# Optimization experiments

Hardware: AMD Instinct MI355X
Metric: run time of the kernel (lower is better)

## Reference

```python
import jax, jax.numpy as jnp
import numpy as np

HEADS = 8
DIM_HEAD = 64
INNER = HEADS * DIM_HEAD  # 512
DIM = 256
MSA_H = 128  # number of MSA rows
MSA_W = 256  # sequence length


def setup_inputs() -> dict:
    key = jax.random.key(0)
    ks = jax.random.split(key, 8)
    n = MSA_H * MSA_W
    w_std = 0.02
    return {
        "x": jax.random.normal(ks[0], (1, n, DIM), dtype=jnp.float32),
        "wq_w": jax.random.normal(ks[1], (DIM, INNER), dtype=jnp.float32) * w_std,
        "wkv_w": jax.random.normal(ks[2], (DIM, 2 * INNER), dtype=jnp.float32) * w_std,
        "wout_w": jax.random.normal(ks[3], (INNER, DIM), dtype=jnp.float32) * w_std,
        "wout_b": jnp.zeros((DIM,), dtype=jnp.float32),
        "hq_w": jax.random.normal(ks[4], (DIM, INNER), dtype=jnp.float32) * w_std,
        "hkv_w": jax.random.normal(ks[5], (DIM, 2 * INNER), dtype=jnp.float32) * w_std,
        "hout_w": jax.random.normal(ks[6], (INNER, DIM), dtype=jnp.float32) * w_std,
        "hout_b": jnp.zeros((DIM,), dtype=jnp.float32),
        "msa_h": MSA_H,
        "msa_w": MSA_W,
    }


def reference(x, wq_w, wkv_w, wout_w, wout_b, hq_w, hkv_w, hout_w, hout_b, msa_h, msa_w):
    b, n, d = x.shape
    h, w = msa_h, msa_w
    scale = DIM_HEAD ** -0.5
    x4 = x.reshape(b, h, w, d)  # (b, rows, cols, dim)

    # ---- width attention: attend across MSA rows (h), independent per column (w) ----
    xw = jnp.swapaxes(x4, 1, 2)  # (b, w, h, d)
    q = (xw @ wq_w).reshape(b, w, h, HEADS, DIM_HEAD)
    kv = (xw @ wkv_w).reshape(b, w, h, 2, HEADS, DIM_HEAD)
    k, v = kv[..., 0, :, :], kv[..., 1, :, :]
    dots = jnp.einsum('bwiHd,bwjHd->bwHij', q, k) * scale  # (b, w, H, h, h)
    attn = jax.nn.softmax(dots, axis=-1)
    o = jnp.einsum('bwHij,bwjHd->bwiHd', attn, v).reshape(b, w, h, INNER)
    w_out = o @ wout_w + wout_b  # (b, w, h, d)
    w_out = jnp.swapaxes(w_out, 1, 2)  # (b, h, w, d)

    # ---- height attention: attend across columns (w), rows tied (tie_attn_dim = h) ----
    q = (x4 @ hq_w).reshape(b, h, w, HEADS, DIM_HEAD)
    kv = (x4 @ hkv_w).reshape(b, h, w, 2, HEADS, DIM_HEAD)
    k, v = kv[..., 0, :, :], kv[..., 1, :, :]
    tie_scale = scale * (h ** -0.5)
    # scores summed over tied row dim r: 'b r h i d, b r h j d -> b h i j'
    dots = jnp.einsum('briHd,brjHd->bHij', q, k) * tie_scale  # (b, H, w, w)
    attn = jax.nn.softmax(dots, axis=-1)
    o = jnp.einsum('bHij,brjHd->briHd', attn, v).reshape(b, h, w, INNER)
    h_out = o @ hout_w + hout_b  # (b, h, w, d)

    out = w_out + h_out
    return out.reshape(b, h * w, d)
```

## Files before the change

kernel.cpp:

```cpp
#include <hip/hip_runtime.h>

typedef short s16x8 __attribute__((ext_vector_type(8)));
typedef float f32x4 __attribute__((ext_vector_type(4)));

#define MFMA16(a, b, c) __builtin_amdgcn_mfma_f32_16x16x32_bf16((a), (b), (c), 0, 0, 0)

__device__ __forceinline__ unsigned short f2b(float f) {
  union { float f; unsigned int u; } v; v.f = f;
  unsigned int u = v.u;
  unsigned int r = (u + 0x7fffu + ((u >> 16) & 1u)) >> 16;
  return (unsigned short)r;
}
__device__ __forceinline__ float b2f(unsigned short b) {
  union { unsigned int u; float f; } v; v.u = ((unsigned int)b) << 16;
  return v.f;
}

__device__ __forceinline__ void gld_lds16(const void* g, void* l) {
  __builtin_amdgcn_global_load_lds(
      (const __attribute__((address_space(1))) unsigned int*)g,
      (__attribute__((address_space(3))) unsigned int*)l, 16, 0, 0);
}

__global__ __launch_bounds__(256) void cvt_x(const float* __restrict__ x,
                                             unsigned short* __restrict__ xb) {
  size_t i = ((size_t)blockIdx.x * 256 + threadIdx.x) * 4;
  float4 v = *(const float4*)(x + i);
  ushort4 o;
  o.x = f2b(v.x); o.y = f2b(v.y); o.z = f2b(v.z); o.w = f2b(v.w);
  *(ushort4*)(xb + i) = o;
}

__global__ __launch_bounds__(256) void build_wt(const float* __restrict__ wq,
                                                const float* __restrict__ wkv,
                                                const float* __restrict__ hq,
                                                const float* __restrict__ hkv,
                                                unsigned short* __restrict__ WT) {
  const int n = blockIdx.x, k = threadIdx.x;
  float v;
  if (n < 512)       v = wq [(size_t)k * 512  + n];
  else if (n < 1536) v = wkv[(size_t)k * 1024 + (n - 512)];
  else if (n < 2048) v = hq [(size_t)k * 512  + (n - 1536)];
  else               v = hkv[(size_t)k * 1024 + (n - 2048)];
  WT[(size_t)n * 256 + k] = f2b(v);
}

__global__ __launch_bounds__(256) void build_w2t(const float* __restrict__ wout,
                                                 const float* __restrict__ hout,
                                                 unsigned short* __restrict__ W2T) {
  const int n = blockIdx.x;
  for (int k = threadIdx.x; k < 1024; k += 256) {
    const float v = (k < 512) ? wout[(size_t)k * 256 + n] : hout[(size_t)(k - 512) * 256 + n];
    W2T[(size_t)n * 1024 + k] = f2b(v);
  }
}

__global__ __launch_bounds__(256) void gemm_qkv(const unsigned short* __restrict__ X,
                                                const unsigned short* __restrict__ WT,
                                                unsigned short* __restrict__ C,
                                                int branch) {
  __shared__ unsigned short As[128 * 32];
  __shared__ unsigned short Bs[128 * 32];
  const int tid = threadIdx.x, wave = tid >> 6, lane = tid & 63;
  const int q = lane >> 4, l = lane & 15;
  const int m0 = blockIdx.x * 128;
  const int n0 = blockIdx.y * 128;
  const int mt = (wave >> 1) * 64;
  const int nt = (wave & 1) * 64;
  const char* Xb = (const char*)X;
  const char* Wb = (const char*)WT;
  const int srow = wave * 32 + (lane >> 2);
  const int sboff = (lane & 3) * 16;
  char* AsB = (char*)As;
  char* BsB = (char*)Bs;
  f32x4 acc[4][4] = {};
#pragma unroll
  for (int ks = 0; ks < 8; ++ks) {
    const int kb = ks * 64;
    gld_lds16(Xb + (size_t)(m0 + srow) * 512 + kb + sboff, AsB + wave * 2048);
    gld_lds16(Xb + (size_t)(m0 + srow + 16) * 512 + kb + sboff, AsB + wave * 2048 + 1024);
    gld_lds16(Wb + (size_t)(n0 + srow) * 512 + kb + sboff, BsB + wave * 2048);
    gld_lds16(Wb + (size_t)(n0 + srow + 16) * 512 + kb + sboff, BsB + wave * 2048 + 1024);
    __syncthreads();
    s16x8 a[4], b[4];
#pragma unroll
    for (int i = 0; i < 4; ++i) a[i] = *(const s16x8*)(&As[(mt + i * 16 + l) * 32 + q * 8]);
#pragma unroll
    for (int j = 0; j < 4; ++j) b[j] = *(const s16x8*)(&Bs[(nt + j * 16 + l) * 32 + q * 8]);
#pragma unroll
    for (int i = 0; i < 4; ++i)
#pragma unroll
      for (int j = 0; j < 4; ++j) acc[i][j] = MFMA16(a[i], b[j], acc[i][j]);
    __syncthreads();
  }
#pragma unroll
  for (int i = 0; i < 4; ++i)
#pragma unroll
    for (int j = 0; j < 4; ++j) {
      const int col = n0 + nt + j * 16 + l;
      const int part = col >> 9, H = (col & 511) >> 6, d = col & 63;
      unsigned short* base = C + (size_t)part * 16777216;
#pragma unroll
      for (int r = 0; r < 4; ++r) {
        const int m = m0 + mt + i * 16 + q * 4 + r;
        size_t idx;
        if (branch == 0) idx = ((size_t)((m & 255) * 8 + H) * 128 + (m >> 8)) * 64 + d;
        else             idx = ((size_t)((m >> 8) * 8 + H) * 256 + (m & 255)) * 64 + d;
        base[idx] = f2b(acc[i][j][r]);
      }
    }
}

__global__ __launch_bounds__(256) void col_attn(const unsigned short* __restrict__ C,
                                                unsigned short* __restrict__ O) {
  __shared__ unsigned short Sp[128 * 136];
  __shared__ unsigned short Vt[64 * 136];
  __shared__ float rowinv[128];
  const int w = blockIdx.x, H = blockIdx.y;
  const int tid = threadIdx.x, wave = tid >> 6, lane = tid & 63;
  const int q = lane >> 4, l = lane & 15;
  const size_t slab = (size_t)(w * 8 + H) * 8192;
  const unsigned short* Qs = C + slab;
  const unsigned short* Ks = C + 16777216 + slab;
  const unsigned short* Vs = C + 33554432 + slab;
  for (int u = tid; u < 1024; u += 256) {
    const int j = u >> 3, db = u & 7;
    s16x8 v = *(const s16x8*)(Vs + j * 64 + db * 8);
#pragma unroll
    for (int t = 0; t < 8; ++t) Vt[(db * 8 + t) * 136 + j] = v[t];
  }
  {
    const int m0 = wave * 32;
    f32x4 acc[2][8] = {};
#pragma unroll
    for (int ks = 0; ks < 2; ++ks) {
      const int kk = ks * 32 + q * 8;
      s16x8 a[2], b[8];
#pragma unroll
      for (int i = 0; i < 2; ++i) a[i] = *(const s16x8*)(Qs + (m0 + i * 16 + l) * 64 + kk);
#pragma unroll
      for (int j = 0; j < 8; ++j) b[j] = *(const s16x8*)(Ks + (j * 16 + l) * 64 + kk);
#pragma unroll
      for (int i = 0; i < 2; ++i)
#pragma unroll
        for (int j = 0; j < 8; ++j) acc[i][j] = MFMA16(a[i], b[j], acc[i][j]);
    }
#pragma unroll
    for (int i = 0; i < 2; ++i)
#pragma unroll
      for (int j = 0; j < 8; ++j)
#pragma unroll
        for (int r = 0; r < 4; ++r)
          Sp[(m0 + i * 16 + q * 4 + r) * 136 + j * 16 + l] = f2b(acc[i][j][r] * 0.125f);
  }
  __syncthreads();
  if (tid < 128) {
    float mx = -1e30f;
    for (int j = 0; j < 128; ++j) mx = fmaxf(mx, b2f(Sp[tid * 136 + j]));
    float s = 0.f;
    for (int j = 0; j < 128; ++j) {
      float e = __expf(b2f(Sp[tid * 136 + j]) - mx);
      s += e;
      Sp[tid * 136 + j] = f2b(e);
    }
    rowinv[tid] = 1.0f / s;
  }
  __syncthreads();
  {
    const int m0 = wave * 32;
    f32x4 acc[2][4] = {};
#pragma unroll
    for (int ks = 0; ks < 4; ++ks) {
      const int kk = ks * 32 + q * 8;
      s16x8 a[2], b[4];
#pragma unroll
      for (int i = 0; i < 2; ++i) a[i] = *(const s16x8*)(&Sp[(m0 + i * 16 + l) * 136 + kk]);
#pragma unroll
      for (int j = 0; j < 4; ++j) b[j] = *(const s16x8*)(&Vt[(j * 16 + l) * 136 + kk]);
#pragma unroll
      for (int i = 0; i < 2; ++i)
#pragma unroll
        for (int j = 0; j < 4; ++j) acc[i][j] = MFMA16(a[i], b[j], acc[i][j]);
    }
#pragma unroll
    for (int i = 0; i < 2; ++i)
#pragma unroll
      for (int j = 0; j < 4; ++j)
#pragma unroll
        for (int r = 0; r < 4; ++r) {
          const int row = m0 + i * 16 + q * 4 + r;
          const int d = j * 16 + l;
          O[(size_t)(row * 256 + w) * 1024 + H * 64 + d] = f2b(acc[i][j][r] * rowinv[row]);
        }
  }
}

__global__ __launch_bounds__(256) void row_dots(const unsigned short* __restrict__ C,
                                                float* __restrict__ dp) {
  const int H = blockIdx.z;
  const int r0 = blockIdx.y * 16;
  const int ti = blockIdx.x & 1, tj = blockIdx.x >> 1;
  const int tid = threadIdx.x, wave = tid >> 6, lane = tid & 63;
  const int q = lane >> 4, l = lane & 15;
  const int m0 = ti * 128 + (wave >> 1) * 64;
  const int n0 = tj * 128 + (wave & 1) * 64;
  const unsigned short* Qh = C;
  const unsigned short* Kh = C + 16777216;
  f32x4 acc[4][4] = {};
  for (int ks = 0; ks < 32; ++ks) {
    const int k = ks * 32 + q * 8;
    const int rr = r0 + (k >> 6), d = k & 63;
    const size_t slab = (size_t)(rr * 8 + H) * 16384;
    s16x8 a[4], b[4];
#pragma unroll
    for (int i = 0; i < 4; ++i) a[i] = *(const s16x8*)(Qh + slab + (m0 + i * 16 + l) * 64 + d);
#pragma unroll
    for (int j = 0; j < 4; ++j) b[j] = *(const s16x8*)(Kh + slab + (n0 + j * 16 + l) * 64 + d);
#pragma unroll
    for (int i = 0; i < 4; ++i)
#pragma unroll
      for (int j = 0; j < 4; ++j) acc[i][j] = MFMA16(a[i], b[j], acc[i][j]);
  }
  float* outp = dp + ((size_t)blockIdx.y * 8 + H) * 65536;
#pragma unroll
  for (int i = 0; i < 4; ++i)
#pragma unroll
    for (int j = 0; j < 4; ++j)
#pragma unroll
      for (int r = 0; r < 4; ++r)
        outp[(size_t)(m0 + i * 16 + q * 4 + r) * 256 + n0 + j * 16 + l] = acc[i][j][r];
}

__global__ __launch_bounds__(256) void row_softmax(const float* __restrict__ dp,
                                                   unsigned short* __restrict__ attn) {
  const int row = blockIdx.x;
  const int H = row >> 8, i = row & 255;
  const int t = threadIdx.x, wave = t >> 6, lane = t & 63;
  __shared__ float red[8];
  float v = 0.f;
#pragma unroll
  for (int c = 0; c < 8; ++c) v += dp[((size_t)c * 8 + H) * 65536 + (size_t)i * 256 + t];
  v *= 1.1048543456e-2f;
  float m = v;
  for (int o = 32; o > 0; o >>= 1) m = fmaxf(m, __shfl_xor(m, o, 64));
  if (lane == 0) red[wave] = m;
  __syncthreads();
  const float M = fmaxf(fmaxf(red[0], red[1]), fmaxf(red[2], red[3]));
  const float e = __expf(v - M);
  float s = e;
  for (int o = 32; o > 0; o >>= 1) s += __shfl_xor(s, o, 64);
  if (lane == 0) red[4 + wave] = s;
  __syncthreads();
  const float S = red[4] + red[5] + red[6] + red[7];
  attn[(size_t)row * 256 + t] = f2b(e / S);
}

__global__ __launch_bounds__(256) void row_pv(const unsigned short* __restrict__ C,
                                              const unsigned short* __restrict__ attn,
                                              unsigned short* __restrict__ O) {
  __shared__ unsigned short Vt[64 * 264];
  const int r = blockIdx.x, H = blockIdx.y;
  const int tid = threadIdx.x, wave = tid >> 6, lane = tid & 63;
  const int q = lane >> 4, l = lane & 15;
  const unsigned short* Vs = C + 33554432 + (size_t)(r * 8 + H) * 16384;
  for (int u = tid; u < 2048; u += 256) {
    const int j = u >> 3, db = u & 7;
    s16x8 v = *(const s16x8*)(Vs + j * 64 + db * 8);
#pragma unroll
    for (int t = 0; t < 8; ++t) Vt[(db * 8 + t) * 264 + j] = v[t];
  }
  __syncthreads();
  const unsigned short* A = attn + (size_t)H * 65536;
  const int m0 = wave * 64;
  f32x4 acc[4][4] = {};
#pragma unroll
  for (int ks = 0; ks < 8; ++ks) {
    const int kk = ks * 32 + q * 8;
    s16x8 a[4], b[4];
#pragma unroll
    for (int i = 0; i < 4; ++i) a[i] = *(const s16x8*)(A + (size_t)(m0 + i * 16 + l) * 256 + kk);
#pragma unroll
    for (int j = 0; j < 4; ++j) b[j] = *(const s16x8*)(&Vt[(j * 16 + l) * 264 + kk]);
#pragma unroll
    for (int i = 0; i < 4; ++i)
#pragma unroll
      for (int j = 0; j < 4; ++j) acc[i][j] = MFMA16(a[i], b[j], acc[i][j]);
  }
#pragma unroll
  for (int i = 0; i < 4; ++i)
#pragma unroll
    for (int j = 0; j < 4; ++j)
#pragma unroll
      for (int rr = 0; rr < 4; ++rr) {
        const int iw = m0 + i * 16 + q * 4 + rr;
        const int d = j * 16 + l;
        O[(size_t)(r * 256 + iw) * 1024 + 512 + H * 64 + d] = f2b(acc[i][j][rr]);
      }
}

__global__ __launch_bounds__(256) void out_proj(const unsigned short* __restrict__ O,
                                                const unsigned short* __restrict__ W2T,
                                                const float* __restrict__ bw,
                                                const float* __restrict__ bh,
                                                float* __restrict__ out) {
  __shared__ unsigned short As[128 * 32];
  __shared__ unsigned short Bs[128 * 32];
  const int tid = threadIdx.x, wave = tid >> 6, lane = tid & 63;
  const int q = lane >> 4, l = lane & 15;
  const int m0 = blockIdx.x * 128;
  const int n0 = blockIdx.y * 128;
  const int mt = (wave >> 1) * 64;
  const int nt = (wave & 1) * 64;
  const char* Ob = (const char*)O;
  const char* Wb = (const char*)W2T;
  const int srow = wave * 32 + (lane >> 2);
  const int sboff = (lane & 3) * 16;
  char* AsB = (char*)As;
  char* BsB = (char*)Bs;
  f32x4 acc[4][4] = {};
  for (int ks = 0; ks < 32; ++ks) {
    const int kb = ks * 64;
    gld_lds16(Ob + (size_t)(m0 + srow) * 2048 + kb + sboff, AsB + wave * 2048);
    gld_lds16(Ob + (size_t)(m0 + srow + 16) * 2048 + kb + sboff, AsB + wave * 2048 + 1024);
    gld_lds16(Wb + (size_t)(n0 + srow) * 2048 + kb + sboff, BsB + wave * 2048);
    gld_lds16(Wb + (size_t)(n0 + srow + 16) * 2048 + kb + sboff, BsB + wave * 2048 + 1024);
    __syncthreads();
    s16x8 a[4], b[4];
#pragma unroll
    for (int i = 0; i < 4; ++i) a[i] = *(const s16x8*)(&As[(mt + i * 16 + l) * 32 + q * 8]);
#pragma unroll
    for (int j = 0; j < 4; ++j) b[j] = *(const s16x8*)(&Bs[(nt + j * 16 + l) * 32 + q * 8]);
#pragma unroll
    for (int i = 0; i < 4; ++i)
#pragma unroll
      for (int j = 0; j < 4; ++j) acc[i][j] = MFMA16(a[i], b[j], acc[i][j]);
    __syncthreads();
  }
#pragma unroll
  for (int i = 0; i < 4; ++i)
#pragma unroll
    for (int j = 0; j < 4; ++j) {
      const int col = n0 + nt + j * 16 + l;
      const float bias = bw[col] + bh[col];
#pragma unroll
      for (int r = 0; r < 4; ++r)
        out[(size_t)(m0 + mt + i * 16 + q * 4 + r) * 256 + col] = acc[i][j][r] + bias;
    }
}

extern "C" void kernel_launch(void* const* d_in, const int* in_sizes, int n_in,
                              void* d_out, int out_size, void* d_ws, size_t ws_size,
                              hipStream_t stream) {
  const float* x    = (const float*)d_in[0];
  const float* wq   = (const float*)d_in[1];
  const float* wkv  = (const float*)d_in[2];
  const float* wout = (const float*)d_in[3];
  const float* bw   = (const float*)d_in[4];
  const float* hq   = (const float*)d_in[5];
  const float* hkv  = (const float*)d_in[6];
  const float* hout = (const float*)d_in[7];
  const float* bh   = (const float*)d_in[8];
  float* out = (float*)d_out;

  char* ws = (char*)d_ws;
  unsigned short* x_bf  = (unsigned short*)(ws);
  unsigned short* WcatT = (unsigned short*)(ws + 16777216);
  unsigned short* W2T   = (unsigned short*)(ws + 18350080);
  float*          dp    = (float*)(ws + 18874368);
  unsigned short* attn  = (unsigned short*)(ws + 35651584);
  unsigned short* Ocat  = (unsigned short*)(ws + 36700160);
  unsigned short* Cproj = (unsigned short*)(ws + 103809024);

  cvt_x<<<8192, 256, 0, stream>>>(x, x_bf);
  build_wt<<<3072, 256, 0, stream>>>(wq, wkv, hq, hkv, WcatT);
  build_w2t<<<256, 256, 0, stream>>>(wout, hout, W2T);

  gemm_qkv<<<dim3(256, 12), 256, 0, stream>>>(x_bf, WcatT, Cproj, 0);
  col_attn<<<dim3(256, 8), 256, 0, stream>>>(Cproj, Ocat);
  gemm_qkv<<<dim3(256, 12), 256, 0, stream>>>(x_bf, WcatT + 1536 * 256, Cproj, 1);
  row_dots<<<dim3(4, 8, 8), 256, 0, stream>>>(Cproj, dp);
  row_softmax<<<2048, 256, 0, stream>>>(dp, attn);
  row_pv<<<dim3(128, 8), 256, 0, stream>>>(Cproj, attn, Ocat);
  out_proj<<<dim3(256, 2), 256, 0, stream>>>(Ocat, W2T, bw, bh, out);
}
```

Before: 364.0 us.

## Pre-transpose V in separate kernel, fuse column softmax into registers, split O buffers

Adds a transpose_v kernel that writes V in d-major layout to global memory, so col_attn and row_pv read B operands directly instead of doing a scattered per-element LDS transpose. The column softmax now runs in registers with cross-lane shuffles, replacing a serial 128-thread pass over LDS, and it normalises before the bf16 cast. The output buffer is split into separate width and height halves, with the workspace reshuffled to alias regions. Two extra launches and extra global traffic for V^T are added in exchange.

```diff
diff --git a/kernel.cpp b/kernel.cpp
--- a/kernel.cpp
+++ b/kernel.cpp
@@ -111,88 +111,108 @@
     }
 }
 
+__global__ __launch_bounds__(256) void transpose_v(const unsigned short* __restrict__ V,
+                                                   unsigned short* __restrict__ VT,
+                                                   int J, int bpsShift) {
+  __shared__ unsigned short T[128 * 72];
+  const int tid = threadIdx.x;
+  const int slab = blockIdx.x >> bpsShift;
+  const int j0 = (blockIdx.x & ((1 << bpsShift) - 1)) * 128;
+  const unsigned short* Vs = V + (size_t)slab * J * 64;
+  unsigned short* VTs = VT + (size_t)slab * J * 64;
+#pragma unroll
+  for (int u = tid; u < 1024; u += 256) {
+    const int j = u >> 3, db = u & 7;
+    s16x8 v = *(const s16x8*)(Vs + (size_t)(j0 + j) * 64 + db * 8);
+    *(s16x8*)(&T[j * 72 + db * 8]) = v;
+  }
+  __syncthreads();
+#pragma unroll
+  for (int it = 0; it < 4; ++it) {
+    const int v = it * 256 + tid;
+    const int d = v & 63, jb = v >> 6;
+    unsigned short tmp[8];
+#pragma unroll
+    for (int t = 0; t < 8; ++t) tmp[t] = T[(jb * 8 + t) * 72 + d];
+    *(s16x8*)(VTs + (size_t)d * J + j0 + jb * 8) = *(s16x8*)tmp;
+  }
+}
+
 __global__ __launch_bounds__(256) void col_attn(const unsigned short* __restrict__ C,
-                                                unsigned short* __restrict__ O) {
+                                                const unsigned short* __restrict__ VT,
+                                                unsigned short* __restrict__ Ow) {
   __shared__ unsigned short Sp[128 * 136];
-  __shared__ unsigned short Vt[64 * 136];
-  __shared__ float rowinv[128];
   const int w = blockIdx.x, H = blockIdx.y;
   const int tid = threadIdx.x, wave = tid >> 6, lane = tid & 63;
   const int q = lane >> 4, l = lane & 15;
   const size_t slab = (size_t)(w * 8 + H) * 8192;
   const unsigned short* Qs = C + slab;
   const unsigned short* Ks = C + 16777216 + slab;
-  const unsigned short* Vs = C + 33554432 + slab;
-  for (int u = tid; u < 1024; u += 256) {
-    const int j = u >> 3, db = u & 7;
-    s16x8 v = *(const s16x8*)(Vs + j * 64 + db * 8);
-#pragma unroll
-    for (int t = 0; t < 8; ++t) Vt[(db * 8 + t) * 136 + j] = v[t];
-  }
-  {
-    const int m0 = wave * 32;
-    f32x4 acc[2][8] = {};
-#pragma unroll
-    for (int ks = 0; ks < 2; ++ks) {
-      const int kk = ks * 32 + q * 8;
-      s16x8 a[2], b[8];
-#pragma unroll
-      for (int i = 0; i < 2; ++i) a[i] = *(const s16x8*)(Qs + (m0 + i * 16 + l) * 64 + kk);
-#pragma unroll
-      for (int j = 0; j < 8; ++j) b[j] = *(const s16x8*)(Ks + (j * 16 + l) * 64 + kk);
-#pragma unroll
-      for (int i = 0; i < 2; ++i)
-#pragma unroll
-        for (int j = 0; j < 8; ++j) acc[i][j] = MFMA16(a[i], b[j], acc[i][j]);
+  const unsigned short* VTs = VT + slab;
+  const int m0 = wave * 32;
+  f32x4 acc[2][8] = {};
+#pragma unroll
+  for (int ks = 0; ks < 2; ++ks) {
+    const int kk = ks * 32 + q * 8;
+    s16x8 a[2], b[8];
+#pragma unroll
+    for (int i = 0; i < 2; ++i) a[i] = *(const s16x8*)(Qs + (m0 + i * 16 + l) * 64 + kk);
+#pragma unroll
+    for (int j = 0; j < 8; ++j) b[j] = *(const s16x8*)(Ks + (j * 16 + l) * 64 + kk);
+#pragma unroll
+    for (int i = 0; i < 2; ++i)
+#pragma unroll
+      for (int j = 0; j < 8; ++j) acc[i][j] = MFMA16(a[i], b[j], acc[i][j]);
+  }
+#pragma unroll
+  for (int i = 0; i < 2; ++i)
+#pragma unroll
+    for (int r = 0; r < 4; ++r) {
+      float vj[8];
+      float mx = -1e30f;
+#pragma unroll
+      for (int j = 0; j < 8; ++j) { vj[j] = acc[i][j][r] * 0.125f; mx = fmaxf(mx, vj[j]); }
+      mx = fmaxf(mx, __shfl_xor(mx, 1, 64));
+      mx = fmaxf(mx, __shfl_xor(mx, 2, 64));
+      mx = fmaxf(mx, __shfl_xor(mx, 4, 64));
+      mx = fmaxf(mx, __shfl_xor(mx, 8, 64));
+      float s = 0.f;
+#pragma unroll
+      for (int j = 0; j < 8; ++j) { vj[j] = __expf(vj[j] - mx); s += vj[j]; }
+      s += __shfl_xor(s, 1, 64);
+      s += __shfl_xor(s, 2, 64);
+      s += __shfl_xor(s, 4, 64);
+      s += __shfl_xor(s, 8, 64);
+      const float inv = 1.0f / s;
+      const int row = m0 + i * 16 + q * 4 + r;
+#pragma unroll
+      for (int j = 0; j < 8; ++j) Sp[row * 136 + j * 16 + l] = f2b(vj[j] * inv);
     }
+  __syncthreads();
+  f32x4 o[2][4] = {};
+#pragma unroll
+  for (int ks = 0; ks < 4; ++ks) {
+    const int kk = ks * 32 + q * 8;
+    s16x8 a[2], b[4];
+#pragma unroll
+    for (int i = 0; i < 2; ++i) a[i] = *(const s16x8*)(&Sp[(m0 + i * 16 + l) * 136 + kk]);
+#pragma unroll
+    for (int j = 0; j < 4; ++j) b[j] = *(const s16x8*)(VTs + (j * 16 + l) * 128 + kk);
 #pragma unroll
     for (int i = 0; i < 2; ++i)
 #pragma unroll
-      for (int j = 0; j < 8; ++j)
-#pragma unroll
-        for (int r = 0; r < 4; ++r)
-          Sp[(m0 + i * 16 + q * 4 + r) * 136 + j * 16 + l] = f2b(acc[i][j][r] * 0.125f);
-  }
-  __syncthreads();
-  if (tid < 128) {
-    float mx = -1e30f;
-    for (int j = 0; j < 128; ++j) mx = fmaxf(mx, b2f(Sp[tid * 136 + j]));
-    float s = 0.f;
-    for (int j = 0; j < 128; ++j) {
-      float e = __expf(b2f(Sp[tid * 136 + j]) - mx);
-      s += e;
-      Sp[tid * 136 + j] = f2b(e);
-    }
-    rowinv[tid] = 1.0f / s;
-  }
-  __syncthreads();
-  {
-    const int m0 = wave * 32;
-    f32x4 acc[2][4] = {};
-#pragma unroll
-    for (int ks = 0; ks < 4; ++ks) {
-      const int kk = ks * 32 + q * 8;
-      s16x8 a[2], b[4];
-#pragma unroll
-      for (int i = 0; i < 2; ++i) a[i] = *(const s16x8*)(&Sp[(m0 + i * 16 + l) * 136 + kk]);
-#pragma unroll
-      for (int j = 0; j < 4; ++j) b[j] = *(const s16x8*)(&Vt[(j * 16 + l) * 136 + kk]);
-#pragma unroll
-      for (int i = 0; i < 2; ++i)
-#pragma unroll
-        for (int j = 0; j < 4; ++j) acc[i][j] = MFMA16(a[i], b[j], acc[i][j]);
-    }
-#pragma unroll
-    for (int i = 0; i < 2; ++i)
-#pragma unroll
-      for (int j = 0; j < 4; ++j)
-#pragma unroll
-        for (int r = 0; r < 4; ++r) {
-          const int row = m0 + i * 16 + q * 4 + r;
-          const int d = j * 16 + l;
-          O[(size_t)(row * 256 + w) * 1024 + H * 64 + d] = f2b(acc[i][j][r] * rowinv[row]);
-        }
-  }
+      for (int j = 0; j < 4; ++j) o[i][j] = MFMA16(a[i], b[j], o[i][j]);
+  }
+#pragma unroll
+  for (int i = 0; i < 2; ++i)
+#pragma unroll
+    for (int j = 0; j < 4; ++j)
+#pragma unroll
+      for (int r = 0; r < 4; ++r) {
+        const int row = m0 + i * 16 + q * 4 + r;
+        const int d = j * 16 + l;
+        Ow[(size_t)(row * 256 + w) * 512 + H * 64 + d] = f2b(o[i][j][r]);
+      }
 }
 
 __global__ __launch_bounds__(256) void row_dots(const unsigned short* __restrict__ C,
@@ -255,21 +275,13 @@
   attn[(size_t)row * 256 + t] = f2b(e / S);
 }
 
-__global__ __launch_bounds__(256) void row_pv(const unsigned short* __restrict__ C,
-                                              const unsigned short* __restrict__ attn,
-                                              unsigned short* __restrict__ O) {
-  __shared__ unsigned short Vt[64 * 264];
+__global__ __launch_bounds__(256) void row_pv(const unsigned short* __restrict__ attn,
+                                              const unsigned short* __restrict__ VT,
+                                              unsigned short* __restrict__ Oh) {
   const int r = blockIdx.x, H = blockIdx.y;
   const int tid = threadIdx.x, wave = tid >> 6, lane = tid & 63;
   const int q = lane >> 4, l = lane & 15;
-  const unsigned short* Vs = C + 33554432 + (size_t)(r * 8 + H) * 16384;
-  for (int u = tid; u < 2048; u += 256) {
-    const int j = u >> 3, db = u & 7;
-    s16x8 v = *(const s16x8*)(Vs + j * 64 + db * 8);
-#pragma unroll
-    for (int t = 0; t < 8; ++t) Vt[(db * 8 + t) * 264 + j] = v[t];
-  }
-  __syncthreads();
+  const unsigned short* VTs = VT + (size_t)(r * 8 + H) * 16384;
   const unsigned short* A = attn + (size_t)H * 65536;
   const int m0 = wave * 64;
   f32x4 acc[4][4] = {};
@@ -280,7 +292,7 @@
 #pragma unroll
     for (int i = 0; i < 4; ++i) a[i] = *(const s16x8*)(A + (size_t)(m0 + i * 16 + l) * 256 + kk);
 #pragma unroll
-    for (int j = 0; j < 4; ++j) b[j] = *(const s16x8*)(&Vt[(j * 16 + l) * 264 + kk]);
+    for (int j = 0; j < 4; ++j) b[j] = *(const s16x8*)(VTs + (j * 16 + l) * 256 + kk);
 #pragma unroll
     for (int i = 0; i < 4; ++i)
 #pragma unroll
@@ -294,11 +306,12 @@
       for (int rr = 0; rr < 4; ++rr) {
         const int iw = m0 + i * 16 + q * 4 + rr;
         const int d = j * 16 + l;
-        O[(size_t)(r * 256 + iw) * 1024 + 512 + H * 64 + d] = f2b(acc[i][j][rr]);
+        Oh[(size_t)(r * 256 + iw) * 512 + H * 64 + d] = f2b(acc[i][j][rr]);
       }
 }
 
-__global__ __launch_bounds__(256) void out_proj(const unsigned short* __restrict__ O,
+__global__ __launch_bounds__(256) void out_proj(const unsigned short* __restrict__ Ow,
+                                                const unsigned short* __restrict__ Oh,
                                                 const unsigned short* __restrict__ W2T,
                                                 const float* __restrict__ bw,
                                                 const float* __restrict__ bh,
@@ -311,7 +324,8 @@
   const int n0 = blockIdx.y * 128;
   const int mt = (wave >> 1) * 64;
   const int nt = (wave & 1) * 64;
-  const char* Ob = (const char*)O;
+  const char* OwB = (const char*)Ow;
+  const char* OhB = (const char*)Oh;
   const char* Wb = (const char*)W2T;
   const int srow = wave * 32 + (lane >> 2);
   const int sboff = (lane & 3) * 16;
@@ -319,11 +333,12 @@
   char* BsB = (char*)Bs;
   f32x4 acc[4][4] = {};
   for (int ks = 0; ks < 32; ++ks) {
-    const int kb = ks * 64;
-    gld_lds16(Ob + (size_t)(m0 + srow) * 2048 + kb + sboff, AsB + wave * 2048);
-    gld_lds16(Ob + (size_t)(m0 + srow + 16) * 2048 + kb + sboff, AsB + wave * 2048 + 1024);
-    gld_lds16(Wb + (size_t)(n0 + srow) * 2048 + kb + sboff, BsB + wave * 2048);
-    gld_lds16(Wb + (size_t)(n0 + srow + 16) * 2048 + kb + sboff, BsB + wave * 2048 + 1024);
+    const char* Ob = (ks < 16) ? OwB : OhB;
+    const int kb = (ks & 15) * 64;
+    gld_lds16(Ob + (size_t)(m0 + srow) * 1024 + kb + sboff, AsB + wave * 2048);
+    gld_lds16(Ob + (size_t)(m0 + srow + 16) * 1024 + kb + sboff, AsB + wave * 2048 + 1024);
+    gld_lds16(Wb + (size_t)(n0 + srow) * 2048 + ks * 64 + sboff, BsB + wave * 2048);
+    gld_lds16(Wb + (size_t)(n0 + srow + 16) * 2048 + ks * 64 + sboff, BsB + wave * 2048 + 1024);
     __syncthreads();
     s16x8 a[4], b[4];
 #pragma unroll
@@ -364,11 +379,14 @@
 
   char* ws = (char*)d_ws;
   unsigned short* x_bf  = (unsigned short*)(ws);
-  unsigned short* WcatT = (unsigned short*)(ws + 16777216);
-  unsigned short* W2T   = (unsigned short*)(ws + 18350080);
-  float*          dp    = (float*)(ws + 18874368);
+  float*          dp    = (float*)(ws + 16777216);
+  unsigned short* VT1   = (unsigned short*)(ws);
+  unsigned short* WcatT = (unsigned short*)(ws + 33554432);
+  unsigned short* W2T   = (unsigned short*)(ws + 35127296);
   unsigned short* attn  = (unsigned short*)(ws + 35651584);
-  unsigned short* Ocat  = (unsigned short*)(ws + 36700160);
+  unsigned short* Ow    = (unsigned short*)(ws + 36700160);
+  unsigned short* Oh    = (unsigned short*)(ws + 70254592);
+  unsigned short* VT0   = Oh;
   unsigned short* Cproj = (unsigned short*)(ws + 103809024);
 
   cvt_x<<<8192, 256, 0, stream>>>(x, x_bf);
@@ -376,10 +394,12 @@
   build_w2t<<<256, 256, 0, stream>>>(wout, hout, W2T);
 
   gemm_qkv<<<dim3(256, 12), 256, 0, stream>>>(x_bf, WcatT, Cproj, 0);
-  col_attn<<<dim3(256, 8), 256, 0, stream>>>(Cproj, Ocat);
+  transpose_v<<<2048, 256, 0, stream>>>(Cproj + (size_t)2 * 16777216, VT0, 128, 0);
+  col_attn<<<dim3(256, 8), 256, 0, stream>>>(Cproj, VT0, Ow);
   gemm_qkv<<<dim3(256, 12), 256, 0, stream>>>(x_bf, WcatT + 1536 * 256, Cproj, 1);
   row_dots<<<dim3(4, 8, 8), 256, 0, stream>>>(Cproj, dp);
   row_softmax<<<2048, 256, 0, stream>>>(dp, attn);
-  row_pv<<<dim3(128, 8), 256, 0, stream>>>(Cproj, attn, Ocat);
-  out_proj<<<dim3(256, 2), 256, 0, stream>>>(Ocat, W2T, bw, bh, out);
-}
+  transpose_v<<<2048, 256, 0, stream>>>(Cproj + (size_t)2 * 16777216, VT1, 256, 1);
+  row_pv<<<dim3(128, 8), 256, 0, stream>>>(attn, VT1, Oh);
+  out_proj<<<dim3(256, 2), 256, 0, stream>>>(Ow, Oh, W2T, bw, bh, out);
+}
```

Result: slower. 397.5 us (+9.2%).
